# Performance work log

Measured on AMD Instinct MI355X. Metric: run time of the kernel, lower is better.

Reference implementation:

```python
import jax, jax.numpy as jnp
import numpy as np


def setup_inputs() -> dict:
    key = jax.random.key(0)
    ks = jax.random.split(key, 7)
    N, D, K = 500000, 128, 32
    return {
        "x": jax.random.normal(ks[0], (N, D), dtype=jnp.float32),
        "h_e": jax.random.normal(ks[1], (N, D), dtype=jnp.float32),
        "bond_n": jax.random.uniform(ks[2], (K, N), dtype=jnp.float32),
        "W_i_w": jax.random.normal(ks[3], (D, 2 * D), dtype=jnp.float32) * 0.05,
        "W_i_b": jax.random.normal(ks[4], (D,), dtype=jnp.float32) * 0.05,
        "W_m_w": jax.random.normal(ks[5], (D, D), dtype=jnp.float32) * 0.05,
        "W_m_b": jax.random.normal(ks[6], (D,), dtype=jnp.float32) * 0.05,
    }


def reference(x, h_e, bond_n, W_i_w, W_i_b, W_m_w, W_m_b):
    # h_n = relu(W_i([x ; h_e]))  -> [N, D]
    h_n = jax.nn.relu(jnp.concatenate([x, h_e], axis=1) @ W_i_w.T + W_i_b)
    # m = sum_k sum_n bond_n[k,n] * h_n[n,:]  -> [D]
    # (equivalent to torch: (bond_n[...,None] * h_n).sum(1).sum(0),
    #  but expressed as a contraction to avoid the [K,N,D] intermediate)
    m = jnp.einsum('kn,nd->d', bond_n, h_n)
    # h = relu(h_n + W_m(m))  -> [N, D] via broadcast of the [D] message
    h = jax.nn.relu(h_n + (m @ W_m_w.T + W_m_b))
    return h
```

## Files before the change

### kernel.cpp

```cpp
#include <hip/hip_runtime.h>
#include <stdint.h>
#include <stddef.h>

#define N_ROWS 500000
#define DDIM   128
#define K2     256
#define KBOND  32
#define TILE2  32
#define NT2    (N_ROWS / TILE2)
#define NB     512
#define P2_BLOCKS 2048

typedef float  f32x4  __attribute__((ext_vector_type(4)));
typedef __bf16 bf16x8 __attribute__((ext_vector_type(8)));
typedef __bf16 bf16x4 __attribute__((ext_vector_type(4)));

__device__ __bf16 g_wbf[DDIM * K2];
__device__ float  g_s[N_ROWS];
__device__ float  g_partials[NB * DDIM];
__device__ float  g_msg[DDIM];
__device__ __bf16 g_hn[(size_t)N_ROWS * DDIM];

__global__ void k_prep(const float* __restrict__ w) {
  int t = blockIdx.x * blockDim.x + threadIdx.x;
  if (t < DDIM * K2) g_wbf[t] = (__bf16)w[t];
}

__global__ __launch_bounds__(256)
void k_s(const float* __restrict__ bond) {
  int n = blockIdx.x * 256 + threadIdx.x;
  if (n >= N_ROWS) return;
  float a = 0.f, b = 0.f;
  #pragma unroll
  for (int k = 0; k < KBOND; k += 2) {
    a += bond[(size_t)k * N_ROWS + n];
    b += bond[(size_t)(k + 1) * N_ROWS + n];
  }
  g_s[n] = a + b;
}

static __device__ __forceinline__ void gload16(const float* g, float* l) {
  __builtin_amdgcn_global_load_lds(
      (const __attribute__((address_space(1))) void*)g,
      (__attribute__((address_space(3))) void*)l, 16, 0, 0);
}

__global__ __launch_bounds__(512, 4)
void k_pass1(const float* __restrict__ x, const float* __restrict__ he,
             const float* __restrict__ bias)
{
  __shared__ float a_lds[2][TILE2 * K2];

  const int tid  = threadIdx.x;
  const int w    = tid >> 6;
  const int lane = tid & 63;
  const int l15  = lane & 15;
  const int g    = lane >> 4;

  bf16x8 wfrag[8];
  #pragma unroll
  for (int ks = 0; ks < 8; ++ks)
    wfrag[ks] = *(const bf16x8*)(g_wbf + (size_t)(16 * w + l15) * K2 + 32 * ks + 8 * g);

  const int d0 = 16 * w + 4 * g;
  const f32x4 bv = *(const f32x4*)(bias + d0);

  const float* sbase = ((lane < 32) ? x : he) + 4 * ((lane & 31) ^ w);

  f32x4 macc = (f32x4)(0.f);

  int t = blockIdx.x;
  {
    const size_t rowb = (size_t)(t * TILE2 + w) * DDIM;
    #pragma unroll
    for (int j = 0; j < 4; ++j)
      gload16(sbase + rowb + (size_t)(8 * j) * DDIM,
              &a_lds[0][(512 * j + 64 * w) * 4]);
  }
  float s0 = g_s[t * TILE2 + l15];
  float s1 = g_s[t * TILE2 + 16 + l15];
  __syncthreads();

  int cur = 0;
  while (true) {
    const int  tn  = t + NB;
    const bool has = tn < NT2;
    float s0n = 0.f, s1n = 0.f;

    if (has) {
      const size_t rowb = (size_t)(tn * TILE2 + w) * DDIM;
      #pragma unroll
      for (int j = 0; j < 4; ++j)
        gload16(sbase + rowb + (size_t)(8 * j) * DDIM,
                &a_lds[cur ^ 1][(512 * j + 64 * w) * 4]);
      s0n = g_s[tn * TILE2 + l15];
      s1n = g_s[tn * TILE2 + 16 + l15];
    }

    f32x4 acc0 = (f32x4)(0.f), acc1 = (f32x4)(0.f);
    const char* base = (const char*)&a_lds[cur][0];
    const int sw = (l15 & 7) << 4;
    #pragma unroll
    for (int ks = 0; ks < 8; ++ks) {
      const int o = 128 * ks + 32 * g;
      f32x4 u0 = *(const f32x4*)(base + l15 * 1024        + ((o)      ^ sw));
      f32x4 u1 = *(const f32x4*)(base + l15 * 1024        + ((o + 16) ^ sw));
      f32x4 v0 = *(const f32x4*)(base + (16 + l15) * 1024 + ((o)      ^ sw));
      f32x4 v1 = *(const f32x4*)(base + (16 + l15) * 1024 + ((o + 16) ^ sw));
      bf16x8 b0, b1;
      #pragma unroll
      for (int i = 0; i < 4; ++i) {
        b0[i] = (__bf16)u0[i]; b0[4 + i] = (__bf16)u1[i];
        b1[i] = (__bf16)v0[i]; b1[4 + i] = (__bf16)v1[i];
      }
      acc0 = __builtin_amdgcn_mfma_f32_16x16x32_bf16(wfrag[ks], b0, acc0, 0, 0, 0);
      acc1 = __builtin_amdgcn_mfma_f32_16x16x32_bf16(wfrag[ks], b1, acc1, 0, 0, 0);
    }

    __syncthreads();

    {
      const int rb = t * TILE2;
      f32x4 h0, h1;
      #pragma unroll
      for (int i = 0; i < 4; ++i) {
        float a = acc0[i] + bv[i]; h0[i] = a > 0.f ? a : 0.f;
        float b = acc1[i] + bv[i]; h1[i] = b > 0.f ? b : 0.f;
      }
      macc += s0 * h0 + s1 * h1;
      bf16x4 hb0, hb1;
      #pragma unroll
      for (int i = 0; i < 4; ++i) { hb0[i] = (__bf16)h0[i]; hb1[i] = (__bf16)h1[i]; }
      *(bf16x4*)(g_hn + (size_t)(rb + l15) * DDIM + d0)      = hb0;
      *(bf16x4*)(g_hn + (size_t)(rb + 16 + l15) * DDIM + d0) = hb1;
    }

    if (!has) break;
    cur ^= 1; t = tn; s0 = s0n; s1 = s1n;
  }

  #pragma unroll
  for (int off = 1; off <= 8; off <<= 1) {
    #pragma unroll
    for (int i = 0; i < 4; ++i) macc[i] += __shfl_xor(macc[i], off, 64);
  }
  if (l15 == 0)
    *(f32x4*)(&g_partials[(size_t)blockIdx.x * DDIM + d0]) = macc;
}

__global__ void k_msg(const float* __restrict__ wm, const float* __restrict__ bm) {
  __shared__ float ms[DDIM];
  __shared__ float sp[DDIM];
  const int d    = threadIdx.x & 127;
  const int half = threadIdx.x >> 7;
  float s = 0.f;
  for (int c = half; c < NB; c += 2) s += g_partials[c * DDIM + d];
  if (half == 0) sp[d] = s;
  __syncthreads();
  if (half == 1) ms[d] = sp[d] + s;
  __syncthreads();
  if (half == 0) {
    float acc = bm[d];
    #pragma unroll 8
    for (int j = 0; j < DDIM; ++j) acc += ms[j] * wm[(size_t)d * DDIM + j];
    g_msg[d] = acc;
  }
}

__global__ __launch_bounds__(256)
void k_pass2(float* __restrict__ out)
{
  __shared__ float ms[DDIM];
  if (threadIdx.x < DDIM) ms[threadIdx.x] = g_msg[threadIdx.x];
  __syncthreads();
  const size_t total = (size_t)N_ROWS * DDIM / 8;
  for (size_t c = (size_t)blockIdx.x * blockDim.x + threadIdx.x; c < total;
       c += (size_t)gridDim.x * blockDim.x) {
    const size_t base = c * 8;
    const int col0 = (int)(base & (DDIM - 1));
    bf16x8 hv = *(const bf16x8*)(g_hn + base);
    f32x4 o0, o1;
    #pragma unroll
    for (int i = 0; i < 4; ++i) {
      float a = (float)hv[i]     + ms[col0 + i];
      float b = (float)hv[4 + i] + ms[col0 + 4 + i];
      o0[i] = a > 0.f ? a : 0.f;
      o1[i] = b > 0.f ? b : 0.f;
    }
    *(f32x4*)(out + base)     = o0;
    *(f32x4*)(out + base + 4) = o1;
  }
}

extern "C" void kernel_launch(void* const* d_in, const int* in_sizes, int n_in,
                              void* d_out, int out_size, void* d_ws, size_t ws_size,
                              hipStream_t stream) {
  const float* x    = (const float*)d_in[0];
  const float* he   = (const float*)d_in[1];
  const float* bond = (const float*)d_in[2];
  const float* wi   = (const float*)d_in[3];
  const float* bi   = (const float*)d_in[4];
  const float* wm   = (const float*)d_in[5];
  const float* bm   = (const float*)d_in[6];
  float* out = (float*)d_out;
  (void)d_ws; (void)ws_size;

  k_prep<<<(DDIM * K2 + 255) / 256, 256, 0, stream>>>(wi);
  k_s<<<(N_ROWS + 255) / 256, 256, 0, stream>>>(bond);
  k_pass1<<<NB, 512, 0, stream>>>(x, he, bi);
  k_msg<<<1, 256, 0, stream>>>(wm, bm);
  k_pass2<<<P2_BLOCKS, 256, 0, stream>>>(out);
}
```

Baseline: 315.8 us.

## Stage bf16 tiles through registers in pass1, triple grid, add two-stage partial reduction

Pass1 no longer uses direct global-to-LDS async loads of fp32. Each thread loads the next tile's x/h_e rows into registers, runs the MFMAs on the current bf16 tile, then converts and writes the prefetched rows to LDS as bf16. This halves LDS footprint and read traffic and removes the per-k-step conversion. The grid grows from 512 to 1536 blocks to raise occupancy, and a new k_mr kernel pre-reduces the larger partials array so k_msg stays short. The cost is more register pressure, an extra launch, and the loss of truly asynchronous LDS loads.

```diff
diff --git a/kernel.cpp b/kernel.cpp
--- a/kernel.cpp
+++ b/kernel.cpp
@@ -6,9 +6,10 @@
 #define DDIM   128
 #define K2     256
 #define KBOND  32
-#define TILE2  32
-#define NT2    (N_ROWS / TILE2)
-#define NB     512
+#define TILE   32
+#define NTL    (N_ROWS / TILE)
+#define NBLK   1536
+#define MR_BLKS 24
 #define P2_BLOCKS 2048
 
 typedef float  f32x4  __attribute__((ext_vector_type(4)));
@@ -17,7 +18,8 @@
 
 __device__ __bf16 g_wbf[DDIM * K2];
 __device__ float  g_s[N_ROWS];
-__device__ float  g_partials[NB * DDIM];
+__device__ float  g_partials[NBLK * DDIM];
+__device__ float  g_p2[MR_BLKS * DDIM];
 __device__ float  g_msg[DDIM];
 __device__ __bf16 g_hn[(size_t)N_ROWS * DDIM];
 
@@ -39,17 +41,11 @@
   g_s[n] = a + b;
 }
 
-static __device__ __forceinline__ void gload16(const float* g, float* l) {
-  __builtin_amdgcn_global_load_lds(
-      (const __attribute__((address_space(1))) void*)g,
-      (__attribute__((address_space(3))) void*)l, 16, 0, 0);
-}
-
-__global__ __launch_bounds__(512, 4)
+__global__ __launch_bounds__(512)
 void k_pass1(const float* __restrict__ x, const float* __restrict__ he,
              const float* __restrict__ bias)
 {
-  __shared__ float a_lds[2][TILE2 * K2];
+  __shared__ __align__(16) unsigned char a_lds[2][TILE * 512];
 
   const int tid  = threadIdx.x;
   const int w    = tid >> 6;
@@ -65,78 +61,92 @@
   const int d0 = 16 * w + 4 * g;
   const f32x4 bv = *(const f32x4*)(bias + d0);
 
-  const float* sbase = ((lane < 32) ? x : he) + 4 * ((lane & 31) ^ w);
+  const int sr = tid >> 4;
+  const int sc = tid & 15;
+  const unsigned swz   = (unsigned)((sr & 15) << 4);
+  const unsigned wo_x  = (unsigned)(sr * 512) + ((16u * sc) ^ swz);
+  const unsigned wo_he = (unsigned)(sr * 512) + 256u + ((16u * sc) ^ swz);
+  const unsigned rsw   = (unsigned)(l15 << 4);
 
   f32x4 macc = (f32x4)(0.f);
 
   int t = blockIdx.x;
+
   {
-    const size_t rowb = (size_t)(t * TILE2 + w) * DDIM;
-    #pragma unroll
-    for (int j = 0; j < 4; ++j)
-      gload16(sbase + rowb + (size_t)(8 * j) * DDIM,
-              &a_lds[0][(512 * j + 64 * w) * 4]);
-  }
-  float s0 = g_s[t * TILE2 + l15];
-  float s1 = g_s[t * TILE2 + 16 + l15];
+    const float* xr = x  + (size_t)(t * TILE + sr) * DDIM + 8 * sc;
+    const float* hr = he + (size_t)(t * TILE + sr) * DDIM + 8 * sc;
+    f32x4 xa = *(const f32x4*)xr, xb = *(const f32x4*)(xr + 4);
+    f32x4 ha = *(const f32x4*)hr, hb = *(const f32x4*)(hr + 4);
+    bf16x8 bx, bh;
+    #pragma unroll
+    for (int i = 0; i < 4; ++i) {
+      bx[i] = (__bf16)xa[i]; bx[4 + i] = (__bf16)xb[i];
+      bh[i] = (__bf16)ha[i]; bh[4 + i] = (__bf16)hb[i];
+    }
+    *(bf16x8*)(&a_lds[0][wo_x])  = bx;
+    *(bf16x8*)(&a_lds[0][wo_he]) = bh;
+  }
+  float s0 = g_s[t * TILE + l15];
+  float s1 = g_s[t * TILE + 16 + l15];
   __syncthreads();
 
   int cur = 0;
   while (true) {
-    const int  tn  = t + NB;
-    const bool has = tn < NT2;
-    float s0n = 0.f, s1n = 0.f;
-
-    if (has) {
-      const size_t rowb = (size_t)(tn * TILE2 + w) * DDIM;
-      #pragma unroll
-      for (int j = 0; j < 4; ++j)
-        gload16(sbase + rowb + (size_t)(8 * j) * DDIM,
-                &a_lds[cur ^ 1][(512 * j + 64 * w) * 4]);
-      s0n = g_s[tn * TILE2 + l15];
-      s1n = g_s[tn * TILE2 + 16 + l15];
-    }
+    const int  tn  = t + NBLK;
+    const bool has = tn < NTL;
+    const int  tl  = has ? tn : t;
+
+    const float* xr = x  + (size_t)(tl * TILE + sr) * DDIM + 8 * sc;
+    const float* hr = he + (size_t)(tl * TILE + sr) * DDIM + 8 * sc;
+    f32x4 xa = *(const f32x4*)xr, xb = *(const f32x4*)(xr + 4);
+    f32x4 ha = *(const f32x4*)hr, hb = *(const f32x4*)(hr + 4);
+    float s0n = g_s[tl * TILE + l15];
+    float s1n = g_s[tl * TILE + 16 + l15];
+    __builtin_amdgcn_sched_barrier(0);
 
     f32x4 acc0 = (f32x4)(0.f), acc1 = (f32x4)(0.f);
-    const char* base = (const char*)&a_lds[cur][0];
-    const int sw = (l15 & 7) << 4;
+    const unsigned char* base = &a_lds[cur][0];
     #pragma unroll
     for (int ks = 0; ks < 8; ++ks) {
-      const int o = 128 * ks + 32 * g;
-      f32x4 u0 = *(const f32x4*)(base + l15 * 1024        + ((o)      ^ sw));
-      f32x4 u1 = *(const f32x4*)(base + l15 * 1024        + ((o + 16) ^ sw));
-      f32x4 v0 = *(const f32x4*)(base + (16 + l15) * 1024 + ((o)      ^ sw));
-      f32x4 v1 = *(const f32x4*)(base + (16 + l15) * 1024 + ((o + 16) ^ sw));
-      bf16x8 b0, b1;
-      #pragma unroll
-      for (int i = 0; i < 4; ++i) {
-        b0[i] = (__bf16)u0[i]; b0[4 + i] = (__bf16)u1[i];
-        b1[i] = (__bf16)v0[i]; b1[4 + i] = (__bf16)v1[i];
-      }
+      const unsigned o = (unsigned)(64 * ks + 16 * g);
+      bf16x8 b0 = *(const bf16x8*)(base + l15 * 512        + (o ^ rsw));
+      bf16x8 b1 = *(const bf16x8*)(base + (16 + l15) * 512 + (o ^ rsw));
       acc0 = __builtin_amdgcn_mfma_f32_16x16x32_bf16(wfrag[ks], b0, acc0, 0, 0, 0);
       acc1 = __builtin_amdgcn_mfma_f32_16x16x32_bf16(wfrag[ks], b1, acc1, 0, 0, 0);
     }
 
-    __syncthreads();
-
     {
-      const int rb = t * TILE2;
+      const int rb = t * TILE;
       f32x4 h0, h1;
       #pragma unroll
       for (int i = 0; i < 4; ++i) {
         float a = acc0[i] + bv[i]; h0[i] = a > 0.f ? a : 0.f;
         float b = acc1[i] + bv[i]; h1[i] = b > 0.f ? b : 0.f;
       }
-      macc += s0 * h0 + s1 * h1;
+      #pragma unroll
+      for (int i = 0; i < 4; ++i) macc[i] += s0 * h0[i] + s1 * h1[i];
       bf16x4 hb0, hb1;
       #pragma unroll
       for (int i = 0; i < 4; ++i) { hb0[i] = (__bf16)h0[i]; hb1[i] = (__bf16)h1[i]; }
       *(bf16x4*)(g_hn + (size_t)(rb + l15) * DDIM + d0)      = hb0;
       *(bf16x4*)(g_hn + (size_t)(rb + 16 + l15) * DDIM + d0) = hb1;
     }
+    __builtin_amdgcn_sched_barrier(0);
+
+    {
+      bf16x8 bx, bh;
+      #pragma unroll
+      for (int i = 0; i < 4; ++i) {
+        bx[i] = (__bf16)xa[i]; bx[4 + i] = (__bf16)xb[i];
+        bh[i] = (__bf16)ha[i]; bh[4 + i] = (__bf16)hb[i];
+      }
+      *(bf16x8*)(&a_lds[cur ^ 1][wo_x])  = bx;
+      *(bf16x8*)(&a_lds[cur ^ 1][wo_he]) = bh;
+    }
+    __syncthreads();
 
     if (!has) break;
-    cur ^= 1; t = tn; s0 = s0n; s1 = s1n;
+    t = tn; cur ^= 1; s0 = s0n; s1 = s1n;
   }
 
   #pragma unroll
@@ -148,23 +158,31 @@
     *(f32x4*)(&g_partials[(size_t)blockIdx.x * DDIM + d0]) = macc;
 }
 
+__global__ void k_mr() {
+  const int d    = threadIdx.x & 127;
+  const int half = threadIdx.x >> 7;
+  const int r0   = blockIdx.x * 64;
+  float acc = 0.f;
+  for (int r = r0 + half; r < r0 + 64; r += 2)
+    acc += g_partials[(size_t)r * DDIM + d];
+  __shared__ float sp[DDIM];
+  if (half == 0) sp[d] = acc;
+  __syncthreads();
+  if (half == 1) g_p2[blockIdx.x * DDIM + d] = sp[d] + acc;
+}
+
 __global__ void k_msg(const float* __restrict__ wm, const float* __restrict__ bm) {
   __shared__ float ms[DDIM];
-  __shared__ float sp[DDIM];
-  const int d    = threadIdx.x & 127;
-  const int half = threadIdx.x >> 7;
+  const int d = threadIdx.x;
   float s = 0.f;
-  for (int c = half; c < NB; c += 2) s += g_partials[c * DDIM + d];
-  if (half == 0) sp[d] = s;
-  __syncthreads();
-  if (half == 1) ms[d] = sp[d] + s;
-  __syncthreads();
-  if (half == 0) {
-    float acc = bm[d];
-    #pragma unroll 8
-    for (int j = 0; j < DDIM; ++j) acc += ms[j] * wm[(size_t)d * DDIM + j];
-    g_msg[d] = acc;
-  }
+  #pragma unroll
+  for (int c = 0; c < MR_BLKS; ++c) s += g_p2[c * DDIM + d];
+  ms[d] = s;
+  __syncthreads();
+  float acc = bm[d];
+  #pragma unroll 8
+  for (int j = 0; j < DDIM; ++j) acc += ms[j] * wm[(size_t)d * DDIM + j];
+  g_msg[d] = acc;
 }
 
 __global__ __launch_bounds__(256)
@@ -207,7 +225,8 @@
 
   k_prep<<<(DDIM * K2 + 255) / 256, 256, 0, stream>>>(wi);
   k_s<<<(N_ROWS + 255) / 256, 256, 0, stream>>>(bond);
-  k_pass1<<<NB, 512, 0, stream>>>(x, he, bi);
-  k_msg<<<1, 256, 0, stream>>>(wm, bm);
+  k_pass1<<<NBLK, 512, 0, stream>>>(x, he, bi);
+  k_mr<<<MR_BLKS, 256, 0, stream>>>();
+  k_msg<<<1, 128, 0, stream>>>(wm, bm);
   k_pass2<<<P2_BLOCKS, 256, 0, stream>>>(out);
 }
```

New measurement: 266.5 us. 15.6% less time.
